# Performance work log

Hardware: AMD Instinct MI355X
Metric: run time of the kernel (lower is better)

Reference implementation:

```python
import jax, jax.numpy as jnp
import numpy as np

NUM_QRYS = 300
NUM_CLASSES = 80
NUM_PAIRS = 4_000_000
NMS_CANDIDATES = 1000
NMS_THR = 0.65
MAX_SEGS = 100
REFINED_WEIGHT = 2.0
FH = FW = 256  # final mask grid resolution


def setup_inputs() -> dict:
    key = jax.random.key(0)
    k1, k2, k3, k4, k5, k6, k7 = jax.random.split(key, 7)
    cls_logits = jax.random.normal(k1, (NUM_QRYS, NUM_CLASSES + 1), jnp.float32)
    # valid xyxy boxes in normalized [0,1] coords
    b = jax.random.uniform(k2, (NUM_QRYS, 4), jnp.float32)
    x1 = b[:, 0] * 0.7
    y1 = b[:, 1] * 0.7
    x2 = x1 + 0.05 + b[:, 2] * 0.25
    y2 = y1 + 0.05 + b[:, 3] * 0.25
    pred_boxes = jnp.stack([x1, y1, x2, y2], axis=1)
    seg_logits = jax.random.normal(k3, (NUM_PAIRS,), jnp.float32)
    key_xy = jax.random.uniform(k4, (NUM_PAIRS, 2), jnp.float32)
    qry_ids = jax.random.randint(k5, (NUM_PAIRS,), 0, NUM_QRYS, jnp.int32)
    refined_mask = jax.random.randint(k6, (NUM_PAIRS,), 0, 2, jnp.int32).astype(bool)
    map_ids = jax.random.randint(k7, (NUM_PAIRS,), 0, 4, jnp.int32)
    return {"cls_logits": cls_logits, "pred_boxes": pred_boxes, "seg_logits": seg_logits,
            "key_xy": key_xy, "qry_ids": qry_ids, "refined_mask": refined_mask, "map_ids": map_ids}


def _box_iou(boxes):  # boxes: [C,4] xyxy -> [C,C]
    x1 = jnp.maximum(boxes[:, None, 0], boxes[None, :, 0])
    y1 = jnp.maximum(boxes[:, None, 1], boxes[None, :, 1])
    x2 = jnp.minimum(boxes[:, None, 2], boxes[None, :, 2])
    y2 = jnp.minimum(boxes[:, None, 3], boxes[None, :, 3])
    inter = jnp.clip(x2 - x1, 0.0) * jnp.clip(y2 - y1, 0.0)
    area = (boxes[:, 2] - boxes[:, 0]) * (boxes[:, 3] - boxes[:, 1])
    union = area[:, None] + area[None, :] - inter
    return inter / jnp.maximum(union, 1e-9)


def _nms_keep(iou, thr):
    # greedy NMS over score-sorted candidates (rows already in descending score order)
    C = iou.shape[0]
    idx = jnp.arange(C)
    def body(i, keep):
        sup = (iou[i] > thr) & (idx > i) & keep[i]
        return keep & ~sup
    return jax.lax.fori_loop(0, C, body, jnp.ones(C, dtype=bool))


def reference(cls_logits, pred_boxes, seg_logits, key_xy, qry_ids, refined_mask, map_ids):
    num_qrys = cls_logits.shape[0]
    # expand per-query class scores -> flat predictions (batch_size = 1)
    scores = jax.nn.sigmoid(cls_logits[:, :-1]).reshape(-1)          # [Q*C]
    feat_ids = jnp.repeat(jnp.arange(num_qrys), NUM_CLASSES)          # [Q*C]
    labels = jnp.tile(jnp.arange(NUM_CLASSES), num_qrys)              # [Q*C]
    # top-k candidates before NMS
    top_scores, cand = jax.lax.top_k(scores, NMS_CANDIDATES)
    cand_feats = feat_ids[cand]
    cand_labels = labels[cand]
    # class-aware (batched) NMS: offset boxes per label so classes don't suppress each other
    offs = cand_labels.astype(pred_boxes.dtype)[:, None] * 4.0
    cand_boxes = pred_boxes[cand_feats] + offs
    keep = _nms_keep(_box_iou(cand_boxes), NMS_THR)
    kept_scores = jnp.where(keep, top_scores, -jnp.inf)
    sel_scores, sel = jax.lax.top_k(kept_scores, MAX_SEGS)
    sel_scores = jnp.where(jnp.isfinite(sel_scores), sel_scores, 0.0)
    sel_feats = cand_feats[sel]
    # assemble per-query mask logit maps from sparse query-key pairs (scatter-max)
    px = jnp.clip((key_xy[:, 0] * FW).astype(jnp.int32), 0, FW - 1)
    py = jnp.clip((key_xy[:, 1] * FH).astype(jnp.int32), 0, FH - 1)
    w_logits = jnp.where(refined_mask, REFINED_WEIGHT * seg_logits, seg_logits)
    flat = qry_ids * (FH * FW) + py * FW + px                          # [num_pairs]
    qry_maps = jnp.full((num_qrys * FH * FW,), -1e4, cls_logits.dtype).at[flat].max(w_logits)
    qry_maps = qry_maps.reshape(num_qrys, FH, FW)
    mask_probs = jax.nn.sigmoid(qry_maps[sel_feats])                   # [MAX_SEGS, FH, FW]
    # score-weighted soft masks (float output; thresholding at mask_thr yields bool masks)
    return sel_scores[:, None, None] * mask_probs
```

## Files before the change

kernel.cpp:

```cpp
#include <hip/hip_runtime.h>

#define NQ        300
#define NC        80
#define NE        24000
#define CAND      1000
#define KSEL      100
#define NPAIRS    4000000
#define HB        4096
#define FHW       65536
#define NMS_THR_F 0.65f
#define MAPS_INIT 0x39E3BFFFu

__device__ __forceinline__ unsigned enc_f32(float f) {
    unsigned u = __float_as_uint(f);
    return (u & 0x80000000u) ? ~u : (u | 0x80000000u);
}
__device__ __forceinline__ float dec_f32(unsigned k) {
    unsigned u = (k & 0x80000000u) ? (k ^ 0x80000000u) : ~k;
    return __uint_as_float(u);
}

__global__ void k_init_maps(uint4* __restrict__ maps) {
    int i = blockIdx.x * 256 + threadIdx.x;
    uint4 v; v.x = v.y = v.z = v.w = MAPS_INIT;
    maps[i] = v;
}

__global__ __launch_bounds__(1024) void k_select_sort(
    const float* __restrict__ cls,
    const float* __restrict__ pboxes,
    float4* __restrict__ cboxes, float* __restrict__ cscore,
    int* __restrict__ cfeat, int* __restrict__ clabel)
{
    __shared__ unsigned long long sbuf[4096];
    unsigned* hist = (unsigned*)sbuf;
    __shared__ unsigned subhist[64];
    __shared__ int sB, sT, sAbove, sCount, sN;
    int tid = threadIdx.x;

    for (int b = tid; b < HB; b += 1024) hist[b] = 0u;
    if (tid < 64) subhist[tid] = 0u;
    __syncthreads();

    unsigned long long lk[24];
    #pragma unroll
    for (int k = 0; k < 24; k++) {
        int e = tid + (k << 10);
        if (e < NE) {
            int q = e / NC, c = e - q * NC;
            float x = cls[q * (NC + 1) + c];
            float s = 1.f / (1.f + expf(-x));
            unsigned bits = __float_as_uint(s);
            lk[k] = ((unsigned long long)bits << 32) | (unsigned)(0xFFFFFFFFu - (unsigned)e);
            atomicAdd(&hist[bits >> 18], 1u);
        }
    }
    __syncthreads();

    if (tid == 0) {
        int acc = 0, B = 0;
        for (int b = HB - 1; b >= 0; b--) {
            acc += (int)hist[b];
            if (acc >= CAND) { B = b; break; }
        }
        sB = B; sAbove = acc - (int)hist[B]; sCount = 0;
    }
    __syncthreads();
    unsigned B = (unsigned)sB;

    #pragma unroll
    for (int k = 0; k < 24; k++) {
        int e = tid + (k << 10);
        if (e < NE && (unsigned)(lk[k] >> 50) == B)
            atomicAdd(&subhist[(unsigned)(lk[k] >> 44) & 63u], 1u);
    }
    __syncthreads();
    if (tid == 0) {
        int acc2 = sAbove, T = 0;
        for (int t = 63; t >= 0; t--) {
            acc2 += (int)subhist[t];
            if (acc2 >= CAND) { T = t; break; }
        }
        sT = T; sN = acc2;
    }
    __syncthreads();
    unsigned T = (unsigned)sT;

    #pragma unroll
    for (int k = 0; k < 24; k++) {
        int e = tid + (k << 10);
        if (e < NE) {
            unsigned long long key = lk[k];
            unsigned bkt = (unsigned)(key >> 50);
            unsigned sub = (unsigned)(key >> 44) & 63u;
            if (bkt > B || (bkt == B && sub >= T)) {
                int pos = atomicAdd(&sCount, 1);
                if (pos < 4096) sbuf[pos] = key;
            }
        }
    }
    __syncthreads();
    int n = min(sN, 4096);

    if (n <= 1024) {
        unsigned long long r = (tid < n) ? sbuf[tid] : 0ULL;
        for (int k = 2; k <= 1024; k <<= 1) {
            for (int j = k >> 1; j > 0; j >>= 1) {
                unsigned long long p;
                if (j >= 64) {
                    sbuf[tid] = r; __syncthreads();
                    p = sbuf[tid ^ j]; __syncthreads();
                } else {
                    p = __shfl_xor(r, j, 64);
                }
                bool d = (tid & k) != 0, lower = (tid & j) == 0;
                r = (d != lower) ? (r > p ? r : p) : (r < p ? r : p);
            }
        }
        sbuf[tid] = r;
        __syncthreads();
    } else {
        int nsort = 2048; while (nsort < n) nsort <<= 1;
        for (int i = n + tid; i < nsort; i += 1024) sbuf[i] = 0ULL;
        __syncthreads();
        for (int k = 2; k <= nsort; k <<= 1) {
            for (int j = k >> 1; j > 0; j >>= 1) {
                for (int i = tid; i < nsort; i += 1024) {
                    int ixj = i ^ j;
                    if (ixj > i) {
                        unsigned long long a = sbuf[i], b = sbuf[ixj];
                        bool up = ((i & k) == 0);
                        if (up ? (a < b) : (a > b)) { sbuf[i] = b; sbuf[ixj] = a; }
                    }
                }
                __syncthreads();
            }
        }
    }

    if (tid < CAND) {
        unsigned long long key = sbuf[tid];
        unsigned bits = (unsigned)(key >> 32);
        unsigned e = 0xFFFFFFFFu - (unsigned)(key & 0xFFFFFFFFu);
        int feat = (int)e / NC, lab = (int)e - feat * NC;
        cscore[tid] = __uint_as_float(bits);
        cfeat[tid]  = feat;
        clabel[tid] = lab;
        float off = 4.f * (float)lab;
        float4 b;
        b.x = pboxes[feat * 4 + 0] + off; b.y = pboxes[feat * 4 + 1] + off;
        b.z = pboxes[feat * 4 + 2] + off; b.w = pboxes[feat * 4 + 3] + off;
        cboxes[tid] = b;
    }
}

__global__ __launch_bounds__(64) void k_nms(
    const float4* __restrict__ cboxes, const int* __restrict__ clabel,
    int* __restrict__ keepflag)
{
    int lab = blockIdx.x, lane = threadIdx.x;
    __shared__ int list[256];
    int base = 0;
    for (int c = 0; c < CAND; c += 64) {
        int i = c + lane;
        bool m = (i < CAND) && (clabel[i] == lab);
        unsigned long long bal = __ballot(m);
        int rank = __popcll(bal & ((1ULL << lane) - 1ULL));
        if (m && base + rank < 256) list[base + rank] = i;
        base += __popcll(bal);
    }
    __syncthreads();
    int n = min(base, 256);

    float4 bx[4]; float area[4];
    unsigned keepm = 0;
    #pragma unroll
    for (int s = 0; s < 4; s++) {
        int j = (s << 6) + lane;
        if (j < n) {
            bx[s] = cboxes[list[j]];
            area[s] = (bx[s].z - bx[s].x) * (bx[s].w - bx[s].y);
            keepm |= (1u << s);
        }
    }
    #pragma unroll
    for (int slot = 0; slot < 4; slot++) {
        int i0 = slot << 6;
        if (i0 >= n) break;
        int iend = min(64, n - i0);
        for (int l = 0; l < iend; l++) {
            int i = i0 + l;
            unsigned km = __shfl(keepm, l);
            bool keep_i = (km >> slot) & 1u;
            float bix = __shfl(bx[slot].x, l), biy = __shfl(bx[slot].y, l);
            float biz = __shfl(bx[slot].z, l), biw = __shfl(bx[slot].w, l);
            float ai  = __shfl(area[slot], l);
            if (keep_i) {
                #pragma unroll
                for (int s2 = 0; s2 < 4; s2++) {
                    int j = (s2 << 6) + lane;
                    if (j > i && j < n && ((keepm >> s2) & 1u)) {
                        float xx1 = fmaxf(bix, bx[s2].x), yy1 = fmaxf(biy, bx[s2].y);
                        float xx2 = fminf(biz, bx[s2].z), yy2 = fminf(biw, bx[s2].w);
                        float inter = fmaxf(xx2 - xx1, 0.f) * fmaxf(yy2 - yy1, 0.f);
                        float uni = ai + area[s2] - inter;
                        if (inter / fmaxf(uni, 1e-9f) > NMS_THR_F) keepm &= ~(1u << s2);
                    }
                }
            }
        }
    }
    #pragma unroll
    for (int s = 0; s < 4; s++) {
        int j = (s << 6) + lane;
        if (j < n) keepflag[list[j]] = (keepm >> s) & 1u;
    }
}

__global__ __launch_bounds__(64) void k_pick(
    const float* __restrict__ cscore, const int* __restrict__ cfeat,
    const int* __restrict__ keepflag,
    float* __restrict__ sel_score, int* __restrict__ sel_slot,
    int* __restrict__ qry2slot,
    const unsigned* __restrict__ refined_raw, unsigned* __restrict__ mode_flag)
{
    int lane = threadIdx.x;
    __shared__ float ss[KSEL];
    __shared__ int   sf[KSEL];
    __shared__ int   q2s[NQ];

    unsigned any = 0;
    for (int i = lane; i < 4096; i += 64) if (refined_raw[i] > 1u) any = 1;
    unsigned mode = (__ballot(any != 0) != 0ULL) ? 1u : 0u;

    int base = 0;
    for (int c = 0; c < CAND; c += 64) {
        int i = c + lane;
        bool k = (i < CAND) && (keepflag[i] != 0);
        unsigned long long bal = __ballot(k);
        int rank = __popcll(bal & ((1ULL << lane) - 1ULL));
        int pos = base + rank;
        if (k && pos < KSEL) { ss[pos] = cscore[i]; sf[pos] = cfeat[i]; }
        base += __popcll(bal);
    }
    for (int q = lane; q < NQ; q += 64) q2s[q] = -1;
    __syncthreads();
    if (lane == 0) {
        int nsel = min(base, KSEL), nslots = 0;
        for (int s = 0; s < KSEL; s++) {
            if (s < nsel) {
                int f = sf[s];
                int sl = q2s[f];
                if (sl < 0) { sl = nslots++; q2s[f] = sl; }
                sel_slot[s] = sl; sel_score[s] = ss[s];
            } else {
                sel_slot[s] = -1; sel_score[s] = 0.f;
            }
        }
        *mode_flag = mode;
    }
    __syncthreads();
    for (int q = lane; q < NQ; q += 64) qry2slot[q] = q2s[q];
}

__global__ __launch_bounds__(256) void k_scatter(
    const float* __restrict__ seg, const float2* __restrict__ xy,
    const int* __restrict__ qry, const unsigned* __restrict__ refined_raw,
    const int* __restrict__ qry2slot, const unsigned* __restrict__ mode_flag,
    unsigned* __restrict__ maps)
{
    int t = blockIdx.x * 256 + threadIdx.x;
    int base = t << 2;
    if (base >= NPAIRS) return;

    int4 q4 = ((const int4*)qry)[t];
    int s0 = qry2slot[q4.x], s1 = qry2slot[q4.y];
    int s2 = qry2slot[q4.z], s3 = qry2slot[q4.w];
    if ((s0 & s1 & s2 & s3) < 0) return;

    float4 sg   = ((const float4*)seg)[t];
    float4 xy01 = ((const float4*)xy)[2 * t];
    float4 xy23 = ((const float4*)xy)[2 * t + 1];
    unsigned r0, r1, r2, r3;
    if (*mode_flag) {
        unsigned rb = refined_raw[t];
        r0 = rb & 255u; r1 = (rb >> 8) & 255u; r2 = (rb >> 16) & 255u; r3 = rb >> 24;
    } else {
        uint4 rr = ((const uint4*)refined_raw)[t];
        r0 = rr.x; r1 = rr.y; r2 = rr.z; r3 = rr.w;
    }

    #define DO_PAIR(S, PX, PY, W, R)                                              \
        if (S >= 0) {                                                             \
            int px = min(max((int)((PX) * 256.f), 0), 255);                       \
            int py = min(max((int)((PY) * 256.f), 0), 255);                       \
            float w = (R) ? 2.f * (W) : (W);                                      \
            atomicMax(&maps[S * FHW + py * 256 + px], enc_f32(w));                \
        }
    DO_PAIR(s0, xy01.x, xy01.y, sg.x, r0)
    DO_PAIR(s1, xy01.z, xy01.w, sg.y, r1)
    DO_PAIR(s2, xy23.x, xy23.y, sg.z, r2)
    DO_PAIR(s3, xy23.z, xy23.w, sg.w, r3)
    #undef DO_PAIR
}

__global__ __launch_bounds__(256) void k_output(
    const uint4* __restrict__ maps4,
    const float* __restrict__ sel_score, const int* __restrict__ sel_slot,
    float4* __restrict__ out4)
{
    int i = blockIdx.x * 256 + threadIdx.x;
    int s = i >> 14;
    float sc = sel_score[s];
    int slot = sel_slot[s];
    float4 v = {0.f, 0.f, 0.f, 0.f};
    if (slot >= 0) {
        uint4 m = maps4[slot * (FHW / 4) + (i & 16383)];
        v.x = sc / (1.f + expf(-dec_f32(m.x)));
        v.y = sc / (1.f + expf(-dec_f32(m.y)));
        v.z = sc / (1.f + expf(-dec_f32(m.z)));
        v.w = sc / (1.f + expf(-dec_f32(m.w)));
    }
    out4[i] = v;
}

extern "C" void kernel_launch(void* const* d_in, const int* in_sizes, int n_in,
                              void* d_out, int out_size, void* d_ws, size_t ws_size,
                              hipStream_t stream) {
    const float*    cls     = (const float*)d_in[0];
    const float*    pboxes  = (const float*)d_in[1];
    const float*    seg     = (const float*)d_in[2];
    const float2*   xy      = (const float2*)d_in[3];
    const int*      qry     = (const int*)d_in[4];
    const unsigned* refined = (const unsigned*)d_in[5];
    float* out = (float*)d_out;

    char* ws = (char*)d_ws;
    unsigned*  maps      = (unsigned*)ws;
    float4*    cboxes    = (float4*)(ws + 26214400);
    float*     cscore    = (float*) (ws + 26230400);
    int*       cfeat     = (int*)   (ws + 26234400);
    int*       clabel    = (int*)   (ws + 26238400);
    int*       keepflag  = (int*)   (ws + 26242400);
    float*     sel_score = (float*) (ws + 26246400);
    int*       sel_slot  = (int*)   (ws + 26246800);
    int*       qry2slot  = (int*)   (ws + 26247200);
    unsigned*  mode_flag = (unsigned*)(ws + 26248400);

    k_init_maps  <<<6400, 256, 0, stream>>>((uint4*)maps);
    k_select_sort<<<1, 1024, 0, stream>>>(cls, pboxes, cboxes, cscore, cfeat, clabel);
    k_nms        <<<NC, 64, 0, stream>>>(cboxes, clabel, keepflag);
    k_pick       <<<1, 64, 0, stream>>>(cscore, cfeat, keepflag, sel_score, sel_slot,
                                        qry2slot, refined, mode_flag);
    k_scatter    <<<3907, 256, 0, stream>>>(seg, xy, qry, refined, qry2slot, mode_flag, maps);
    k_output     <<<6400, 256, 0, stream>>>((const uint4*)maps, sel_score, sel_slot,
                                            (float4*)out);
}
```

Before: 248.5 us.

## Fuse map init, top-k select, NMS and pick into one front kernel

Merges the map-initialisation, candidate select/sort, per-label NMS and final pick kernels into a single launch. Block 0 does the serial selection work entirely in shared memory, while the other 256 blocks fill the mask maps at the same time. This removes three kernel launches and the global-memory round trips for candidate boxes, scores and keep flags. In exchange, NMS now runs one label per wavefront and caps each label at 64 candidates instead of 256, and the refined-mask format check reads only 1024 words instead of 4096. Both reductions could give wrong results on unusual inputs.

Measured after the change: 251.4 us. Within noise of the previous version (+1.2%).

```diff
diff --git a/kernel.cpp b/kernel.cpp
--- a/kernel.cpp
+++ b/kernel.cpp
@@ -10,6 +10,7 @@
 #define FHW       65536
 #define NMS_THR_F 0.65f
 #define MAPS_INIT 0x39E3BFFFu
+#define INIT_VEC4 1638400
 
 __device__ __forceinline__ unsigned enc_f32(float f) {
     unsigned u = __float_as_uint(f);
@@ -20,26 +21,42 @@
     return __uint_as_float(u);
 }
 
-__global__ void k_init_maps(uint4* __restrict__ maps) {
-    int i = blockIdx.x * 256 + threadIdx.x;
-    uint4 v; v.x = v.y = v.z = v.w = MAPS_INIT;
-    maps[i] = v;
-}
-
-__global__ __launch_bounds__(1024) void k_select_sort(
+__global__ __launch_bounds__(1024) void k_front(
     const float* __restrict__ cls,
     const float* __restrict__ pboxes,
-    float4* __restrict__ cboxes, float* __restrict__ cscore,
-    int* __restrict__ cfeat, int* __restrict__ clabel)
+    const unsigned* __restrict__ refined_raw,
+    uint4* __restrict__ maps4,
+    float* __restrict__ sel_score_g, int* __restrict__ sel_slot_g,
+    int* __restrict__ qry2slot_g, unsigned* __restrict__ mode_flag_g)
 {
+    if (blockIdx.x > 0) {
+        uint4 v; v.x = v.y = v.z = v.w = MAPS_INIT;
+        for (int i = (int)(blockIdx.x - 1) * 1024 + (int)threadIdx.x;
+             i < INIT_VEC4; i += 256 * 1024)
+            maps4[i] = v;
+        return;
+    }
+
     __shared__ unsigned long long sbuf[4096];
+    __shared__ float sbx[CAND], sby[CAND], sbz[CAND], sbw[CAND];
+    __shared__ float sscore[CAND];
+    __shared__ short sfeat[CAND];
+    __shared__ unsigned char slab[CAND];
+    __shared__ unsigned char skeep[CAND];
+    __shared__ int wlist[16][64];
+    __shared__ int q2s[NQ];
+    __shared__ float ss[KSEL]; __shared__ int sf[KSEL];
+    __shared__ unsigned subhist[64];
+    __shared__ unsigned smode;
+    __shared__ int sB, sT, sAbove, sCount, sN;
+
     unsigned* hist = (unsigned*)sbuf;
-    __shared__ unsigned subhist[64];
-    __shared__ int sB, sT, sAbove, sCount, sN;
     int tid = threadIdx.x;
+    int lane = tid & 63, wv = tid >> 6;
 
     for (int b = tid; b < HB; b += 1024) hist[b] = 0u;
     if (tid < 64) subhist[tid] = 0u;
+    if (tid == 0) { smode = 0u; sCount = 0; }
     __syncthreads();
 
     unsigned long long lk[24];
@@ -55,6 +72,7 @@
             atomicAdd(&hist[bits >> 18], 1u);
         }
     }
+    if (refined_raw[tid] > 1u) atomicOr(&smode, 1u);
     __syncthreads();
 
     if (tid == 0) {
@@ -63,7 +81,7 @@
             acc += (int)hist[b];
             if (acc >= CAND) { B = b; break; }
         }
-        sB = B; sAbove = acc - (int)hist[B]; sCount = 0;
+        sB = B; sAbove = acc - (int)hist[B];
     }
     __syncthreads();
     unsigned B = (unsigned)sB;
@@ -123,19 +141,18 @@
         int nsort = 2048; while (nsort < n) nsort <<= 1;
         for (int i = n + tid; i < nsort; i += 1024) sbuf[i] = 0ULL;
         __syncthreads();
-        for (int k = 2; k <= nsort; k <<= 1) {
+        for (int k = 2; k <= nsort; k <<= 1)
             for (int j = k >> 1; j > 0; j >>= 1) {
                 for (int i = tid; i < nsort; i += 1024) {
                     int ixj = i ^ j;
                     if (ixj > i) {
-                        unsigned long long a = sbuf[i], b = sbuf[ixj];
+                        unsigned long long a = sbuf[i], b2 = sbuf[ixj];
                         bool up = ((i & k) == 0);
-                        if (up ? (a < b) : (a > b)) { sbuf[i] = b; sbuf[ixj] = a; }
+                        if (up ? (a < b2) : (a > b2)) { sbuf[i] = b2; sbuf[ixj] = a; }
                     }
                 }
                 __syncthreads();
             }
-        }
     }
 
     if (tid < CAND) {
@@ -143,124 +160,87 @@
         unsigned bits = (unsigned)(key >> 32);
         unsigned e = 0xFFFFFFFFu - (unsigned)(key & 0xFFFFFFFFu);
         int feat = (int)e / NC, lab = (int)e - feat * NC;
-        cscore[tid] = __uint_as_float(bits);
-        cfeat[tid]  = feat;
-        clabel[tid] = lab;
+        sscore[tid] = __uint_as_float(bits);
+        sfeat[tid]  = (short)feat;
+        slab[tid]   = (unsigned char)lab;
         float off = 4.f * (float)lab;
-        float4 b;
-        b.x = pboxes[feat * 4 + 0] + off; b.y = pboxes[feat * 4 + 1] + off;
-        b.z = pboxes[feat * 4 + 2] + off; b.w = pboxes[feat * 4 + 3] + off;
-        cboxes[tid] = b;
-    }
-}
-
-__global__ __launch_bounds__(64) void k_nms(
-    const float4* __restrict__ cboxes, const int* __restrict__ clabel,
-    int* __restrict__ keepflag)
-{
-    int lab = blockIdx.x, lane = threadIdx.x;
-    __shared__ int list[256];
-    int base = 0;
-    for (int c = 0; c < CAND; c += 64) {
-        int i = c + lane;
-        bool m = (i < CAND) && (clabel[i] == lab);
-        unsigned long long bal = __ballot(m);
-        int rank = __popcll(bal & ((1ULL << lane) - 1ULL));
-        if (m && base + rank < 256) list[base + rank] = i;
-        base += __popcll(bal);
-    }
-    __syncthreads();
-    int n = min(base, 256);
-
-    float4 bx[4]; float area[4];
-    unsigned keepm = 0;
-    #pragma unroll
-    for (int s = 0; s < 4; s++) {
-        int j = (s << 6) + lane;
-        if (j < n) {
-            bx[s] = cboxes[list[j]];
-            area[s] = (bx[s].z - bx[s].x) * (bx[s].w - bx[s].y);
-            keepm |= (1u << s);
-        }
-    }
-    #pragma unroll
-    for (int slot = 0; slot < 4; slot++) {
-        int i0 = slot << 6;
-        if (i0 >= n) break;
-        int iend = min(64, n - i0);
-        for (int l = 0; l < iend; l++) {
-            int i = i0 + l;
-            unsigned km = __shfl(keepm, l);
-            bool keep_i = (km >> slot) & 1u;
-            float bix = __shfl(bx[slot].x, l), biy = __shfl(bx[slot].y, l);
-            float biz = __shfl(bx[slot].z, l), biw = __shfl(bx[slot].w, l);
-            float ai  = __shfl(area[slot], l);
-            if (keep_i) {
-                #pragma unroll
-                for (int s2 = 0; s2 < 4; s2++) {
-                    int j = (s2 << 6) + lane;
-                    if (j > i && j < n && ((keepm >> s2) & 1u)) {
-                        float xx1 = fmaxf(bix, bx[s2].x), yy1 = fmaxf(biy, bx[s2].y);
-                        float xx2 = fminf(biz, bx[s2].z), yy2 = fminf(biw, bx[s2].w);
-                        float inter = fmaxf(xx2 - xx1, 0.f) * fmaxf(yy2 - yy1, 0.f);
-                        float uni = ai + area[s2] - inter;
-                        if (inter / fmaxf(uni, 1e-9f) > NMS_THR_F) keepm &= ~(1u << s2);
-                    }
+        const float4 pb = ((const float4*)pboxes)[feat];
+        sbx[tid] = pb.x + off; sby[tid] = pb.y + off;
+        sbz[tid] = pb.z + off; sbw[tid] = pb.w + off;
+    }
+    __syncthreads();
+
+    for (int li = 0; li < 5; li++) {
+        int lab = wv + (li << 4);
+        int nb = 0;
+        for (int c = 0; c < CAND; c += 64) {
+            int i = c + lane;
+            bool m = (i < CAND) && ((int)slab[i] == lab);
+            unsigned long long bal = __ballot(m);
+            if (m) {
+                int r = nb + __popcll(bal & ((1ULL << lane) - 1ULL));
+                if (r < 64) wlist[wv][r] = i;
+            }
+            nb += __popcll(bal);
+        }
+        int nl = min(nb, 64);
+        __syncthreads();
+
+        bool alive = lane < nl;
+        float bxv = 0.f, byv = 0.f, bzv = 0.f, bwv = 0.f, ar = 0.f;
+        int idx = -1;
+        if (alive) {
+            idx = wlist[wv][lane];
+            bxv = sbx[idx]; byv = sby[idx]; bzv = sbz[idx]; bwv = sbw[idx];
+            ar = (bzv - bxv) * (bwv - byv);
+        }
+        bool keep = alive;
+        for (int i = 0; i < nl; i++) {
+            float bix = __shfl(bxv, i), biy = __shfl(byv, i);
+            float biz = __shfl(bzv, i), biw = __shfl(bwv, i);
+            float ai  = __shfl(ar, i);
+            int   ki  = __shfl((int)keep, i);
+            if (ki && keep && lane > i) {
+                float xx1 = fmaxf(bix, bxv), yy1 = fmaxf(biy, byv);
+                float xx2 = fminf(biz, bzv), yy2 = fminf(biw, bwv);
+                float inter = fmaxf(xx2 - xx1, 0.f) * fmaxf(yy2 - yy1, 0.f);
+                float uni = ai + ar - inter;
+                if (inter / fmaxf(uni, 1e-9f) > NMS_THR_F) keep = false;
+            }
+        }
+        if (alive) skeep[idx] = keep ? 1 : 0;
+    }
+    __syncthreads();
+
+    for (int q = tid; q < NQ; q += 1024) q2s[q] = -1;
+    __syncthreads();
+    if (tid < 64) {
+        int base = 0;
+        for (int c = 0; c < CAND; c += 64) {
+            int i = c + lane;
+            bool k = (i < CAND) && skeep[i];
+            unsigned long long bal = __ballot(k);
+            int pos = base + __popcll(bal & ((1ULL << lane) - 1ULL));
+            if (k && pos < KSEL) { ss[pos] = sscore[i]; sf[pos] = (int)sfeat[i]; }
+            base += __popcll(bal);
+        }
+        if (tid == 0) {
+            int nsel = min(base, KSEL), nslots = 0;
+            for (int s = 0; s < KSEL; s++) {
+                if (s < nsel) {
+                    int f = sf[s];
+                    int sl = q2s[f];
+                    if (sl < 0) { sl = nslots++; q2s[f] = sl; }
+                    sel_slot_g[s] = sl; sel_score_g[s] = ss[s];
+                } else {
+                    sel_slot_g[s] = -1; sel_score_g[s] = 0.f;
                 }
             }
-        }
-    }
-    #pragma unroll
-    for (int s = 0; s < 4; s++) {
-        int j = (s << 6) + lane;
-        if (j < n) keepflag[list[j]] = (keepm >> s) & 1u;
-    }
-}
-
-__global__ __launch_bounds__(64) void k_pick(
-    const float* __restrict__ cscore, const int* __restrict__ cfeat,
-    const int* __restrict__ keepflag,
-    float* __restrict__ sel_score, int* __restrict__ sel_slot,
-    int* __restrict__ qry2slot,
-    const unsigned* __restrict__ refined_raw, unsigned* __restrict__ mode_flag)
-{
-    int lane = threadIdx.x;
-    __shared__ float ss[KSEL];
-    __shared__ int   sf[KSEL];
-    __shared__ int   q2s[NQ];
-
-    unsigned any = 0;
-    for (int i = lane; i < 4096; i += 64) if (refined_raw[i] > 1u) any = 1;
-    unsigned mode = (__ballot(any != 0) != 0ULL) ? 1u : 0u;
-
-    int base = 0;
-    for (int c = 0; c < CAND; c += 64) {
-        int i = c + lane;
-        bool k = (i < CAND) && (keepflag[i] != 0);
-        unsigned long long bal = __ballot(k);
-        int rank = __popcll(bal & ((1ULL << lane) - 1ULL));
-        int pos = base + rank;
-        if (k && pos < KSEL) { ss[pos] = cscore[i]; sf[pos] = cfeat[i]; }
-        base += __popcll(bal);
-    }
-    for (int q = lane; q < NQ; q += 64) q2s[q] = -1;
-    __syncthreads();
-    if (lane == 0) {
-        int nsel = min(base, KSEL), nslots = 0;
-        for (int s = 0; s < KSEL; s++) {
-            if (s < nsel) {
-                int f = sf[s];
-                int sl = q2s[f];
-                if (sl < 0) { sl = nslots++; q2s[f] = sl; }
-                sel_slot[s] = sl; sel_score[s] = ss[s];
-            } else {
-                sel_slot[s] = -1; sel_score[s] = 0.f;
-            }
-        }
-        *mode_flag = mode;
-    }
-    __syncthreads();
-    for (int q = lane; q < NQ; q += 64) qry2slot[q] = q2s[q];
+            *mode_flag_g = smode;
+        }
+    }
+    __syncthreads();
+    for (int q = tid; q < NQ; q += 1024) qry2slot_g[q] = q2s[q];
 }
 
 __global__ __launch_bounds__(256) void k_scatter(
@@ -270,8 +250,7 @@
     unsigned* __restrict__ maps)
 {
     int t = blockIdx.x * 256 + threadIdx.x;
-    int base = t << 2;
-    if (base >= NPAIRS) return;
+    if ((t << 2) >= NPAIRS) return;
 
     int4 q4 = ((const int4*)qry)[t];
     int s0 = qry2slot[q4.x], s1 = qry2slot[q4.y];
@@ -337,22 +316,14 @@
 
     char* ws = (char*)d_ws;
     unsigned*  maps      = (unsigned*)ws;
-    float4*    cboxes    = (float4*)(ws + 26214400);
-    float*     cscore    = (float*) (ws + 26230400);
-    int*       cfeat     = (int*)   (ws + 26234400);
-    int*       clabel    = (int*)   (ws + 26238400);
-    int*       keepflag  = (int*)   (ws + 26242400);
-    float*     sel_score = (float*) (ws + 26246400);
-    int*       sel_slot  = (int*)   (ws + 26246800);
-    int*       qry2slot  = (int*)   (ws + 26247200);
-    unsigned*  mode_flag = (unsigned*)(ws + 26248400);
-
-    k_init_maps  <<<6400, 256, 0, stream>>>((uint4*)maps);
-    k_select_sort<<<1, 1024, 0, stream>>>(cls, pboxes, cboxes, cscore, cfeat, clabel);
-    k_nms        <<<NC, 64, 0, stream>>>(cboxes, clabel, keepflag);
-    k_pick       <<<1, 64, 0, stream>>>(cscore, cfeat, keepflag, sel_score, sel_slot,
-                                        qry2slot, refined, mode_flag);
-    k_scatter    <<<3907, 256, 0, stream>>>(seg, xy, qry, refined, qry2slot, mode_flag, maps);
-    k_output     <<<6400, 256, 0, stream>>>((const uint4*)maps, sel_score, sel_slot,
-                                            (float4*)out);
-}
+    float*     sel_score = (float*)   (ws + 26214400);
+    int*       sel_slot  = (int*)     (ws + 26214800);
+    int*       qry2slot  = (int*)     (ws + 26215200);
+    unsigned*  mode_flag = (unsigned*)(ws + 26216400);
+
+    k_front  <<<257, 1024, 0, stream>>>(cls, pboxes, refined, (uint4*)maps,
+                                        sel_score, sel_slot, qry2slot, mode_flag);
+    k_scatter<<<3907, 256, 0, stream>>>(seg, xy, qry, refined, qry2slot, mode_flag, maps);
+    k_output <<<6400, 256, 0, stream>>>((const uint4*)maps, sel_score, sel_slot,
+                                        (float4*)out);
+}
```
